# Kernel tuning notes

Measured on AMD Instinct MI355X. Metric: run time of the kernel, lower is better.

## Reference

```python
import jax, jax.numpy as jnp
import numpy as np


def setup_inputs() -> dict:
    key = jax.random.key(0)
    ks = jax.random.split(key, 7)
    B, EN, DE, E, U, T = 8, 512, 64, 512, 512, 100  # batch, max_words, max_label, emb, units, topics
    return {
        "en_seq": jax.random.normal(ks[0], (B, EN, E), dtype=jnp.float32),
        "de_seq": jax.random.normal(ks[1], (B, DE, E), dtype=jnp.float32),
        "topics": jax.random.uniform(ks[2], (B, T), dtype=jnp.float32),
        "w_en": jax.random.normal(ks[3], (E, U), dtype=jnp.float32) * 0.05,
        "w_de": jax.random.normal(ks[4], (E, U), dtype=jnp.float32) * 0.05,
        "nu": jax.random.normal(ks[5], (U,), dtype=jnp.float32) * 0.05,
        "wt": jax.random.normal(ks[6], (E, T), dtype=jnp.float32) * 0.05,
    }


def reference(en_seq, de_seq, topics, w_en, w_de, nu, wt):
    # Additive (Bahdanau-style) attention with a per-batch topic bias.
    att_en = jnp.einsum("bie,eu->biu", en_seq, w_en)        # [B, EN, U]
    att_de = jnp.einsum("bje,eu->bju", de_seq, w_de)        # [B, DE, U]
    topics_w = jnp.einsum("bt,ut->bu", topics, wt)          # [B, U] (wt is [E,U-dim? no: E==U])
    # co_m[b, j, i, u] = att_en[b,i,u] + att_de[b,j,u] + topics_w[b,u]
    co_m = jnp.tanh(att_en[:, None, :, :] + att_de[:, :, None, :]
                    + topics_w[:, None, None, :])           # [B, DE, EN, U]
    mu = jnp.einsum("bjiu,u->bji", co_m, nu)                # [B, DE, EN]
    alphas = jax.nn.softmax(mu, axis=-1)                    # softmax over encoder positions
    p_gen = jax.nn.sigmoid(mu)
    sum_en = jnp.einsum("bji,bie->bje", alphas, en_seq)     # attention-weighted encoder sum
    output = de_seq + sum_en
    return (output, alphas, p_gen)
```

## Files before the change

### kernel.cpp

```cpp
#include <hip/hip_runtime.h>
#include <hip/hip_bf16.h>

#define NB  8
#define ENW 512
#define DEW 64
#define EMB 512
#define UN  512
#define NT  100

#define KSCALE 2.8853900817779268f
#define L2E    1.4426950408889634f

typedef short bf16x8 __attribute__((ext_vector_type(8)));
typedef unsigned short u16x8 __attribute__((ext_vector_type(8)));
typedef float f32x4  __attribute__((ext_vector_type(4)));

__device__ __forceinline__ unsigned short f2bf(float f) {
    union { float f; unsigned int u; } v; v.f = f;
    unsigned int r = v.u + 0x7FFFu + ((v.u >> 16) & 1u);
    return (unsigned short)(r >> 16);
}

__device__ __forceinline__ float rlane(float v, int l) {
    return __int_as_float(__builtin_amdgcn_readlane(__float_as_int(v), l));
}

__global__ __launch_bounds__(256) void prep_kernel(const float* __restrict__ w_en,
                                                   const float* __restrict__ w_de,
                                                   const float* __restrict__ en,
                                                   const float* __restrict__ de,
                                                   const float* __restrict__ topics,
                                                   const float* __restrict__ wt_mat,
                                                   const float* __restrict__ nu,
                                                   unsigned short* __restrict__ wen_t,
                                                   unsigned short* __restrict__ wde_t,
                                                   unsigned short* __restrict__ en_bf,
                                                   unsigned short* __restrict__ de_bf,
                                                   float* __restrict__ tw2,
                                                   float* __restrict__ snu,
                                                   float* __restrict__ nu2) {
    const int bx = blockIdx.x, t = threadIdx.x;
    if (bx < 128) {
        __shared__ float tile[64][65];
        const float* w = (bx < 64) ? w_en : w_de;
        unsigned short* o = (bx < 64) ? wen_t : wde_t;
        const int tb = bx & 63;
        const int r0 = (tb >> 3) * 64;
        const int c0 = (tb & 7) * 64;
        const int rr = t >> 4, cc = (t & 15) * 4;
#pragma unroll
        for (int q = 0; q < 4; ++q) {
            float4 v = *(const float4*)(w + (size_t)(r0 + rr + 16 * q) * 512 + c0 + cc);
            *(float4*)&tile[rr + 16 * q][cc] = v;
        }
        __syncthreads();
#pragma unroll
        for (int q = 0; q < 4; ++q) {
            int ul = rr + 16 * q;
            int el = cc;
            ushort4 v;
            v.x = f2bf(KSCALE * tile[el][ul]);
            v.y = f2bf(KSCALE * tile[el + 1][ul]);
            v.z = f2bf(KSCALE * tile[el + 2][ul]);
            v.w = f2bf(KSCALE * tile[el + 3][ul]);
            *(ushort4*)(o + (size_t)(c0 + ul) * 512 + r0 + el) = v;
        }
    } else if (bx < 1280) {
        const bool is_en = (bx < 1152);
        const float* src = is_en ? en : de;
        unsigned short* dst = is_en ? en_bf : de_bf;
        const int idx = ((is_en ? (bx - 128) : (bx - 1152)) * 256 + t) * 8;
        float4 a0 = *(const float4*)(src + idx);
        float4 a1 = *(const float4*)(src + idx + 4);
        u16x8 o;
        o[0] = f2bf(a0.x); o[1] = f2bf(a0.y); o[2] = f2bf(a0.z); o[3] = f2bf(a0.w);
        o[4] = f2bf(a1.x); o[5] = f2bf(a1.y); o[6] = f2bf(a1.z); o[7] = f2bf(a1.w);
        *(u16x8*)(dst + idx) = o;
    } else if (bx < 1296) {
        int idx = (bx - 1280) * 256 + t;
        int b = idx >> 9, u = idx & 511;
        const float* tp = topics + b * NT;
        const float* wp = wt_mat + u * NT;
        float s = 0.f;
        for (int tt = 0; tt < NT; ++tt) s += tp[tt] * wp[tt];
        tw2[idx] = KSCALE * s;
    } else {
        __shared__ float red[256];
        float n0 = nu[t], n1 = nu[t + 256];
        nu2[t] = -2.f * n0;
        nu2[t + 256] = -2.f * n1;
        red[t] = n0 + n1;
        __syncthreads();
        for (int off = 128; off > 0; off >>= 1) {
            if (t < off) red[t] += red[t + off];
            __syncthreads();
        }
        if (t == 0) snu[0] = red[0];
    }
}

__global__ __launch_bounds__(256) void gemm_fused(const unsigned short* __restrict__ en_bf,
                                                  const unsigned short* __restrict__ de_bf,
                                                  const unsigned short* __restrict__ wen_t,
                                                  const unsigned short* __restrict__ wde_t,
                                                  const float* __restrict__ tw2,
                                                  float* __restrict__ att_en2,
                                                  float* __restrict__ bias2) {
    const int K = 512, N = 512;
    const int bx = blockIdx.x;
    const bool is_de = (bx >= 64);
    const unsigned short* A = is_de ? de_bf : en_bf;
    const unsigned short* Bt = is_de ? wde_t : wen_t;
    float* C = is_de ? bias2 : att_en2;
    const int mb = is_de ? (bx - 64) : bx;

    const int lane = threadIdx.x & 63;
    const int wave = threadIdx.x >> 6;
    const int m0 = mb * 64 + wave * 16;
    const int n0 = blockIdx.y * 64;
    const int row = m0 + (lane & 15);
    const int kq  = (lane >> 4) * 8;

    f32x4 acc[4];
#pragma unroll
    for (int nn = 0; nn < 4; ++nn) acc[nn] = 0.f;

    const unsigned short* ap = A + (size_t)row * K + kq;
    const unsigned short* bp = Bt + (size_t)(n0 + (lane & 15)) * K + kq;
#pragma unroll 4
    for (int kc = 0; kc < K; kc += 32) {
        bf16x8 a = *(const bf16x8*)(ap + kc);
#pragma unroll
        for (int nn = 0; nn < 4; ++nn) {
            bf16x8 b = *(const bf16x8*)(bp + (size_t)nn * 16 * K + kc);
            acc[nn] = __builtin_amdgcn_mfma_f32_16x16x32_bf16(a, b, acc[nn], 0, 0, 0);
        }
    }
    const int crow = m0 + (lane >> 4) * 4;
    const int ccol = lane & 15;
#pragma unroll
    for (int nn = 0; nn < 4; ++nn)
#pragma unroll
        for (int r = 0; r < 4; ++r) {
            int rw = crow + r, cl = n0 + nn * 16 + ccol;
            float v = acc[nn][r];
            if (is_de) v += tw2[(rw >> 6) * 512 + cl];
            C[(size_t)rw * N + cl] = v;
        }
}

__global__ __launch_bounds__(256) void mu3_kernel(const float* __restrict__ att_en2,
                                                  const float* __restrict__ bias2,
                                                  const float* __restrict__ nu2,
                                                  const float* __restrict__ snu,
                                                  float* __restrict__ mu) {
    __shared__ float As[16][132];
    __shared__ float Bs[16][132];
    __shared__ float Ns[128];
    const int t = threadIdx.x;
    const int bx = blockIdx.x;
    const int jg = bx & 3;
    const int isplit = (bx >> 2) & 31;
    const int b = bx >> 7;
    const int i0 = isplit * 16, j0 = jg * 16;
    const int il = t & 15, jr = t >> 4;

    const float* aeb = att_en2 + (size_t)(b * ENW + i0) * UN;
    const float* bib = bias2 + (size_t)(b * DEW + j0) * UN;

    float s0 = 0.f, s1 = 0.f;
    for (int uc = 0; uc < 512; uc += 128) {
#pragma unroll
        for (int q = 0; q < 2; ++q) {
            int idx = q * 256 + t;
            int row = idx >> 5, c4 = idx & 31;
            float4 va = *(const float4*)(aeb + (size_t)row * UN + uc + c4 * 4);
            *(float4*)&As[row][c4 * 4] = va;
            float4 vb = *(const float4*)(bib + (size_t)row * UN + uc + c4 * 4);
            *(float4*)&Bs[row][c4 * 4] = vb;
        }
        if (t < 32) *(float4*)&Ns[t * 4] = *(const float4*)(nu2 + uc + t * 4);
        __syncthreads();
#pragma unroll 8
        for (int c = 0; c < 32; ++c) {
            float4 a  = *(const float4*)&As[il][c * 4];
            float4 bb = *(const float4*)&Bs[jr][c * 4];
            float4 nv = *(const float4*)&Ns[c * 4];
            float e0 = __builtin_amdgcn_exp2f(a.x + bb.x);
            float e1 = __builtin_amdgcn_exp2f(a.y + bb.y);
            float e2 = __builtin_amdgcn_exp2f(a.z + bb.z);
            float e3 = __builtin_amdgcn_exp2f(a.w + bb.w);
            s0 = fmaf(nv.x, __builtin_amdgcn_rcpf(e0 + 1.f), s0);
            s1 = fmaf(nv.y, __builtin_amdgcn_rcpf(e1 + 1.f), s1);
            s0 = fmaf(nv.z, __builtin_amdgcn_rcpf(e2 + 1.f), s0);
            s1 = fmaf(nv.w, __builtin_amdgcn_rcpf(e3 + 1.f), s1);
        }
        __syncthreads();
    }
    mu[(size_t)(b * DEW + j0 + jr) * ENW + i0 + il] = snu[0] + s0 + s1;
}

__global__ __launch_bounds__(256) void softmax_kernel(const float* __restrict__ mu,
                                                      float* __restrict__ alphas,
                                                      float* __restrict__ p_gen) {
    const int bj = blockIdx.x;
    const float* mup = mu + (size_t)bj * ENW;
    const int t = threadIdx.x;
    float v0 = mup[t], v1 = mup[t + 256];

    float m = fmaxf(v0, v1);
#pragma unroll
    for (int off = 32; off > 0; off >>= 1) m = fmaxf(m, __shfl_xor(m, off));
    __shared__ float wmax[4];
    if ((t & 63) == 0) wmax[t >> 6] = m;
    __syncthreads();
    m = fmaxf(fmaxf(wmax[0], wmax[1]), fmaxf(wmax[2], wmax[3]));

    float e0 = __builtin_amdgcn_exp2f((v0 - m) * L2E);
    float e1 = __builtin_amdgcn_exp2f((v1 - m) * L2E);
    float s = e0 + e1;
#pragma unroll
    for (int off = 32; off > 0; off >>= 1) s += __shfl_xor(s, off);
    __shared__ float wsum[4];
    if ((t & 63) == 0) wsum[t >> 6] = s;
    __syncthreads();
    s = wsum[0] + wsum[1] + wsum[2] + wsum[3];
    float inv = __builtin_amdgcn_rcpf(s);

    alphas[(size_t)bj * ENW + t]       = e0 * inv;
    alphas[(size_t)bj * ENW + t + 256] = e1 * inv;
    p_gen[(size_t)bj * ENW + t]        = __builtin_amdgcn_rcpf(1.f + __builtin_amdgcn_exp2f(-v0 * L2E));
    p_gen[(size_t)bj * ENW + t + 256]  = __builtin_amdgcn_rcpf(1.f + __builtin_amdgcn_exp2f(-v1 * L2E));
}

__global__ __launch_bounds__(64) void outsum_kernel(const float* __restrict__ alphas,
                                                    const float* __restrict__ en,
                                                    float* __restrict__ partial) {
    const int bx = blockIdx.x;
    const int iq = bx & 3;
    const int eh = (bx >> 2) & 1;
    const int jq = (bx >> 3) & 15;
    const int b  = bx >> 7;
    const int lane = threadIdx.x;
    const int i0 = iq * 128, j0 = jq * 4;

    float2 av[4];
#pragma unroll
    for (int jj = 0; jj < 4; ++jj)
        av[jj] = *(const float2*)(alphas + (size_t)(b * DEW + j0 + jj) * ENW + i0 + lane * 2);

    const float* enb = en + (size_t)b * ENW * EMB + eh * 256 + lane * 4;
    f32x4 acc[4];
#pragma unroll
    for (int jj = 0; jj < 4; ++jj) acc[jj] = 0.f;

#pragma unroll 4
    for (int k2 = 0; k2 < 64; ++k2) {
        float4 x0 = *(const float4*)(enb + (size_t)(i0 + 2 * k2) * EMB);
        float4 x1 = *(const float4*)(enb + (size_t)(i0 + 2 * k2 + 1) * EMB);
#pragma unroll
        for (int jj = 0; jj < 4; ++jj) {
            float w0 = rlane(av[jj].x, k2);
            float w1 = rlane(av[jj].y, k2);
            acc[jj][0] = fmaf(w0, x0.x, fmaf(w1, x1.x, acc[jj][0]));
            acc[jj][1] = fmaf(w0, x0.y, fmaf(w1, x1.y, acc[jj][1]));
            acc[jj][2] = fmaf(w0, x0.z, fmaf(w1, x1.z, acc[jj][2]));
            acc[jj][3] = fmaf(w0, x0.w, fmaf(w1, x1.w, acc[jj][3]));
        }
    }
#pragma unroll
    for (int jj = 0; jj < 4; ++jj) {
        float* pp = partial + (size_t)iq * 262144
                  + (size_t)(b * DEW + j0 + jj) * EMB + eh * 256 + lane * 4;
        *(f32x4*)pp = acc[jj];
    }
}

__global__ __launch_bounds__(256) void finout_kernel(const float* __restrict__ partial,
                                                     const float* __restrict__ de,
                                                     float* __restrict__ out) {
    const int idx = (blockIdx.x * 256 + threadIdx.x) * 4;
    float4 d  = *(const float4*)(de + idx);
    float4 p0 = *(const float4*)(partial + idx);
    float4 p1 = *(const float4*)(partial + 262144 + idx);
    float4 p2 = *(const float4*)(partial + 524288 + idx);
    float4 p3 = *(const float4*)(partial + 786432 + idx);
    float4 o;
    o.x = d.x + (p0.x + p1.x) + (p2.x + p3.x);
    o.y = d.y + (p0.y + p1.y) + (p2.y + p3.y);
    o.z = d.z + (p0.z + p1.z) + (p2.z + p3.z);
    o.w = d.w + (p0.w + p1.w) + (p2.w + p3.w);
    *(float4*)(out + idx) = o;
}

extern "C" void kernel_launch(void* const* d_in, const int* in_sizes, int n_in,
                              void* d_out, int out_size, void* d_ws, size_t ws_size,
                              hipStream_t stream) {
    const float* en     = (const float*)d_in[0];
    const float* de     = (const float*)d_in[1];
    const float* topics = (const float*)d_in[2];
    const float* w_en   = (const float*)d_in[3];
    const float* w_de   = (const float*)d_in[4];
    const float* nu     = (const float*)d_in[5];
    const float* wt     = (const float*)d_in[6];

    float* out    = (float*)d_out;
    float* alphas = out + 262144;
    float* p_gen  = out + 524288;

    char* ws = (char*)d_ws;
    float* att_en2        = (float*)(ws);
    float* bias2          = (float*)(ws + 8388608);
    float* tw2            = (float*)(ws + 9437184);
    float* mu             = (float*)(ws + 9453568);
    unsigned short* en_bf = (unsigned short*)(ws + 10502144);
    unsigned short* de_bf = (unsigned short*)(ws + 14696448);
    unsigned short* wen_t = (unsigned short*)(ws + 15220736);
    unsigned short* wde_t = (unsigned short*)(ws + 15745024);
    float* snu            = (float*)(ws + 16269312);
    float* nu2            = (float*)(ws + 16269328);
    float* partial        = (float*)(ws + 16777216);

    prep_kernel<<<1297, 256, 0, stream>>>(w_en, w_de, en, de, topics, wt, nu,
                                          wen_t, wde_t, en_bf, de_bf, tw2, snu, nu2);
    gemm_fused<<<dim3(72, 8), 256, 0, stream>>>(en_bf, de_bf, wen_t, wde_t, tw2,
                                                att_en2, bias2);
    mu3_kernel<<<1024, 256, 0, stream>>>(att_en2, bias2, nu2, snu, mu);
    softmax_kernel<<<512, 256, 0, stream>>>(mu, alphas, p_gen);
    outsum_kernel<<<1024, 64, 0, stream>>>(alphas, en, partial);
    finout_kernel<<<256, 256, 0, stream>>>(partial, de, out);
}
```

Before: 150.0 us.

## Factor exp out of mu inner loop and fuse softmax with weighted sum

The GEMM epilogue now stores exp2 of the scaled projections, so the mu inner loop evaluates tanh through exp(a)*exp(b)+1 with one FMA instead of an add and an exp per element. Softmax, p_gen, the alpha-weighted encoder sum and the de_seq residual are merged into one kernel that keeps alphas in shared memory, which removes the partial buffer and two launches. The factored exponentials can overflow to inf for large inputs, but rcp of inf still gives the correct limit. The fused kernel launches only 256 blocks, so there is less parallelism in the weighted-sum stage.

New measurement: 141.4 us. 1.06x faster.

```diff
diff --git a/kernel.cpp b/kernel.cpp
--- a/kernel.cpp
+++ b/kernel.cpp
@@ -104,14 +104,14 @@
                                                   const unsigned short* __restrict__ wen_t,
                                                   const unsigned short* __restrict__ wde_t,
                                                   const float* __restrict__ tw2,
-                                                  float* __restrict__ att_en2,
-                                                  float* __restrict__ bias2) {
+                                                  float* __restrict__ Ea,
+                                                  float* __restrict__ Eb) {
     const int K = 512, N = 512;
     const int bx = blockIdx.x;
     const bool is_de = (bx >= 64);
     const unsigned short* A = is_de ? de_bf : en_bf;
     const unsigned short* Bt = is_de ? wde_t : wen_t;
-    float* C = is_de ? bias2 : att_en2;
+    float* C = is_de ? Eb : Ea;
     const int mb = is_de ? (bx - 64) : bx;
 
     const int lane = threadIdx.x & 63;
@@ -145,12 +145,12 @@
             int rw = crow + r, cl = n0 + nn * 16 + ccol;
             float v = acc[nn][r];
             if (is_de) v += tw2[(rw >> 6) * 512 + cl];
-            C[(size_t)rw * N + cl] = v;
-        }
-}
-
-__global__ __launch_bounds__(256) void mu3_kernel(const float* __restrict__ att_en2,
-                                                  const float* __restrict__ bias2,
+            C[(size_t)rw * N + cl] = __builtin_amdgcn_exp2f(v);
+        }
+}
+
+__global__ __launch_bounds__(256) void mu4_kernel(const float* __restrict__ Ea,
+                                                  const float* __restrict__ Eb,
                                                   const float* __restrict__ nu2,
                                                   const float* __restrict__ snu,
                                                   float* __restrict__ mu) {
@@ -165,8 +165,8 @@
     const int i0 = isplit * 16, j0 = jg * 16;
     const int il = t & 15, jr = t >> 4;
 
-    const float* aeb = att_en2 + (size_t)(b * ENW + i0) * UN;
-    const float* bib = bias2 + (size_t)(b * DEW + j0) * UN;
+    const float* aeb = Ea + (size_t)(b * ENW + i0) * UN;
+    const float* bib = Eb + (size_t)(b * DEW + j0) * UN;
 
     float s0 = 0.f, s1 = 0.f;
     for (int uc = 0; uc < 512; uc += 128) {
@@ -186,111 +186,118 @@
             float4 a  = *(const float4*)&As[il][c * 4];
             float4 bb = *(const float4*)&Bs[jr][c * 4];
             float4 nv = *(const float4*)&Ns[c * 4];
-            float e0 = __builtin_amdgcn_exp2f(a.x + bb.x);
-            float e1 = __builtin_amdgcn_exp2f(a.y + bb.y);
-            float e2 = __builtin_amdgcn_exp2f(a.z + bb.z);
-            float e3 = __builtin_amdgcn_exp2f(a.w + bb.w);
-            s0 = fmaf(nv.x, __builtin_amdgcn_rcpf(e0 + 1.f), s0);
-            s1 = fmaf(nv.y, __builtin_amdgcn_rcpf(e1 + 1.f), s1);
-            s0 = fmaf(nv.z, __builtin_amdgcn_rcpf(e2 + 1.f), s0);
-            s1 = fmaf(nv.w, __builtin_amdgcn_rcpf(e3 + 1.f), s1);
+            float e0 = fmaf(a.x, bb.x, 1.f);
+            float e1 = fmaf(a.y, bb.y, 1.f);
+            float e2 = fmaf(a.z, bb.z, 1.f);
+            float e3 = fmaf(a.w, bb.w, 1.f);
+            s0 = fmaf(nv.x, __builtin_amdgcn_rcpf(e0), s0);
+            s1 = fmaf(nv.y, __builtin_amdgcn_rcpf(e1), s1);
+            s0 = fmaf(nv.z, __builtin_amdgcn_rcpf(e2), s0);
+            s1 = fmaf(nv.w, __builtin_amdgcn_rcpf(e3), s1);
         }
         __syncthreads();
     }
     mu[(size_t)(b * DEW + j0 + jr) * ENW + i0 + il] = snu[0] + s0 + s1;
 }
 
-__global__ __launch_bounds__(256) void softmax_kernel(const float* __restrict__ mu,
+__global__ __launch_bounds__(256) void softfin_kernel(const float* __restrict__ mu,
+                                                      const float* __restrict__ en,
+                                                      const float* __restrict__ de,
+                                                      float* __restrict__ out,
                                                       float* __restrict__ alphas,
                                                       float* __restrict__ p_gen) {
-    const int bj = blockIdx.x;
-    const float* mup = mu + (size_t)bj * ENW;
+    __shared__ float Al[4][512];
+    __shared__ float Ps[4][4][256];
+    const int bx = blockIdx.x;
+    const int eh = bx & 1;
+    const int jq = (bx >> 1) & 15;
+    const int b  = bx >> 5;
     const int t = threadIdx.x;
-    float v0 = mup[t], v1 = mup[t + 256];
-
-    float m = fmaxf(v0, v1);
-#pragma unroll
-    for (int off = 32; off > 0; off >>= 1) m = fmaxf(m, __shfl_xor(m, off));
-    __shared__ float wmax[4];
-    if ((t & 63) == 0) wmax[t >> 6] = m;
+    const int wave = t >> 6, lane = t & 63;
+    const int j0 = jq * 4;
+
+    {
+        const int bj = b * DEW + j0 + wave;
+        const float* mup = mu + (size_t)bj * ENW;
+        float v[8], a[8];
+#pragma unroll
+        for (int c = 0; c < 8; ++c) v[c] = mup[c * 64 + lane];
+        float mx = v[0];
+#pragma unroll
+        for (int c = 1; c < 8; ++c) mx = fmaxf(mx, v[c]);
+#pragma unroll
+        for (int off = 32; off > 0; off >>= 1) mx = fmaxf(mx, __shfl_xor(mx, off));
+        float s = 0.f;
+#pragma unroll
+        for (int c = 0; c < 8; ++c) { a[c] = __builtin_amdgcn_exp2f((v[c] - mx) * L2E); s += a[c]; }
+#pragma unroll
+        for (int off = 32; off > 0; off >>= 1) s += __shfl_xor(s, off);
+        float inv = __builtin_amdgcn_rcpf(s);
+#pragma unroll
+        for (int c = 0; c < 8; ++c) {
+            a[c] *= inv;
+            Al[wave][c * 64 + lane] = a[c];
+        }
+        if (eh == 0) {
+            float* alp = alphas + (size_t)bj * ENW;
+            float* pgp = p_gen + (size_t)bj * ENW;
+#pragma unroll
+            for (int c = 0; c < 8; ++c) {
+                alp[c * 64 + lane] = a[c];
+                pgp[c * 64 + lane] = __builtin_amdgcn_rcpf(1.f + __builtin_amdgcn_exp2f(-v[c] * L2E));
+            }
+        }
+    }
     __syncthreads();
-    m = fmaxf(fmaxf(wmax[0], wmax[1]), fmaxf(wmax[2], wmax[3]));
-
-    float e0 = __builtin_amdgcn_exp2f((v0 - m) * L2E);
-    float e1 = __builtin_amdgcn_exp2f((v1 - m) * L2E);
-    float s = e0 + e1;
-#pragma unroll
-    for (int off = 32; off > 0; off >>= 1) s += __shfl_xor(s, off);
-    __shared__ float wsum[4];
-    if ((t & 63) == 0) wsum[t >> 6] = s;
-    __syncthreads();
-    s = wsum[0] + wsum[1] + wsum[2] + wsum[3];
-    float inv = __builtin_amdgcn_rcpf(s);
-
-    alphas[(size_t)bj * ENW + t]       = e0 * inv;
-    alphas[(size_t)bj * ENW + t + 256] = e1 * inv;
-    p_gen[(size_t)bj * ENW + t]        = __builtin_amdgcn_rcpf(1.f + __builtin_amdgcn_exp2f(-v0 * L2E));
-    p_gen[(size_t)bj * ENW + t + 256]  = __builtin_amdgcn_rcpf(1.f + __builtin_amdgcn_exp2f(-v1 * L2E));
-}
-
-__global__ __launch_bounds__(64) void outsum_kernel(const float* __restrict__ alphas,
-                                                    const float* __restrict__ en,
-                                                    float* __restrict__ partial) {
-    const int bx = blockIdx.x;
-    const int iq = bx & 3;
-    const int eh = (bx >> 2) & 1;
-    const int jq = (bx >> 3) & 15;
-    const int b  = bx >> 7;
-    const int lane = threadIdx.x;
-    const int i0 = iq * 128, j0 = jq * 4;
-
-    float2 av[4];
-#pragma unroll
-    for (int jj = 0; jj < 4; ++jj)
-        av[jj] = *(const float2*)(alphas + (size_t)(b * DEW + j0 + jj) * ENW + i0 + lane * 2);
-
+
+    const int i0 = wave * 128;
     const float* enb = en + (size_t)b * ENW * EMB + eh * 256 + lane * 4;
     f32x4 acc[4];
 #pragma unroll
     for (int jj = 0; jj < 4; ++jj) acc[jj] = 0.f;
-
-#pragma unroll 4
-    for (int k2 = 0; k2 < 64; ++k2) {
-        float4 x0 = *(const float4*)(enb + (size_t)(i0 + 2 * k2) * EMB);
-        float4 x1 = *(const float4*)(enb + (size_t)(i0 + 2 * k2 + 1) * EMB);
-#pragma unroll
-        for (int jj = 0; jj < 4; ++jj) {
-            float w0 = rlane(av[jj].x, k2);
-            float w1 = rlane(av[jj].y, k2);
-            acc[jj][0] = fmaf(w0, x0.x, fmaf(w1, x1.x, acc[jj][0]));
-            acc[jj][1] = fmaf(w0, x0.y, fmaf(w1, x1.y, acc[jj][1]));
-            acc[jj][2] = fmaf(w0, x0.z, fmaf(w1, x1.z, acc[jj][2]));
-            acc[jj][3] = fmaf(w0, x0.w, fmaf(w1, x1.w, acc[jj][3]));
-        }
-    }
-#pragma unroll
-    for (int jj = 0; jj < 4; ++jj) {
-        float* pp = partial + (size_t)iq * 262144
-                  + (size_t)(b * DEW + j0 + jj) * EMB + eh * 256 + lane * 4;
-        *(f32x4*)pp = acc[jj];
-    }
-}
-
-__global__ __launch_bounds__(256) void finout_kernel(const float* __restrict__ partial,
-                                                     const float* __restrict__ de,
-                                                     float* __restrict__ out) {
-    const int idx = (blockIdx.x * 256 + threadIdx.x) * 4;
-    float4 d  = *(const float4*)(de + idx);
-    float4 p0 = *(const float4*)(partial + idx);
-    float4 p1 = *(const float4*)(partial + 262144 + idx);
-    float4 p2 = *(const float4*)(partial + 524288 + idx);
-    float4 p3 = *(const float4*)(partial + 786432 + idx);
-    float4 o;
-    o.x = d.x + (p0.x + p1.x) + (p2.x + p3.x);
-    o.y = d.y + (p0.y + p1.y) + (p2.y + p3.y);
-    o.z = d.z + (p0.z + p1.z) + (p2.z + p3.z);
-    o.w = d.w + (p0.w + p1.w) + (p2.w + p3.w);
-    *(float4*)(out + idx) = o;
+    for (int ig = 0; ig < 128; ig += 4) {
+        const int ib = i0 + ig;
+        float4 al0 = *(const float4*)&Al[0][ib];
+        float4 al1 = *(const float4*)&Al[1][ib];
+        float4 al2 = *(const float4*)&Al[2][ib];
+        float4 al3 = *(const float4*)&Al[3][ib];
+#pragma unroll
+        for (int r = 0; r < 4; ++r) {
+            float4 x = *(const float4*)(enb + (size_t)(ib + r) * EMB);
+            float w0 = (r == 0) ? al0.x : (r == 1) ? al0.y : (r == 2) ? al0.z : al0.w;
+            float w1 = (r == 0) ? al1.x : (r == 1) ? al1.y : (r == 2) ? al1.z : al1.w;
+            float w2 = (r == 0) ? al2.x : (r == 1) ? al2.y : (r == 2) ? al2.z : al2.w;
+            float w3 = (r == 0) ? al3.x : (r == 1) ? al3.y : (r == 2) ? al3.z : al3.w;
+            acc[0][0] = fmaf(w0, x.x, acc[0][0]); acc[0][1] = fmaf(w0, x.y, acc[0][1]);
+            acc[0][2] = fmaf(w0, x.z, acc[0][2]); acc[0][3] = fmaf(w0, x.w, acc[0][3]);
+            acc[1][0] = fmaf(w1, x.x, acc[1][0]); acc[1][1] = fmaf(w1, x.y, acc[1][1]);
+            acc[1][2] = fmaf(w1, x.z, acc[1][2]); acc[1][3] = fmaf(w1, x.w, acc[1][3]);
+            acc[2][0] = fmaf(w2, x.x, acc[2][0]); acc[2][1] = fmaf(w2, x.y, acc[2][1]);
+            acc[2][2] = fmaf(w2, x.z, acc[2][2]); acc[2][3] = fmaf(w2, x.w, acc[2][3]);
+            acc[3][0] = fmaf(w3, x.x, acc[3][0]); acc[3][1] = fmaf(w3, x.y, acc[3][1]);
+            acc[3][2] = fmaf(w3, x.z, acc[3][2]); acc[3][3] = fmaf(w3, x.w, acc[3][3]);
+        }
+    }
+#pragma unroll
+    for (int jj = 0; jj < 4; ++jj)
+        *(f32x4*)&Ps[wave][jj][lane * 4] = acc[jj];
+    __syncthreads();
+
+    {
+        const int bj = b * DEW + j0 + wave;
+        const int e = eh * 256 + lane * 4;
+        float4 p0 = *(const float4*)&Ps[0][wave][lane * 4];
+        float4 p1 = *(const float4*)&Ps[1][wave][lane * 4];
+        float4 p2 = *(const float4*)&Ps[2][wave][lane * 4];
+        float4 p3 = *(const float4*)&Ps[3][wave][lane * 4];
+        float4 d = *(const float4*)(de + (size_t)bj * EMB + e);
+        float4 o;
+        o.x = d.x + (p0.x + p1.x) + (p2.x + p3.x);
+        o.y = d.y + (p0.y + p1.y) + (p2.y + p3.y);
+        o.z = d.z + (p0.z + p1.z) + (p2.z + p3.z);
+        o.w = d.w + (p0.w + p1.w) + (p2.w + p3.w);
+        *(float4*)(out + (size_t)bj * EMB + e) = o;
+    }
 }
 
 extern "C" void kernel_launch(void* const* d_in, const int* in_sizes, int n_in,
@@ -309,8 +316,8 @@
     float* p_gen  = out + 524288;
 
     char* ws = (char*)d_ws;
-    float* att_en2        = (float*)(ws);
-    float* bias2          = (float*)(ws + 8388608);
+    float* Ea             = (float*)(ws);
+    float* Eb             = (float*)(ws + 8388608);
     float* tw2            = (float*)(ws + 9437184);
     float* mu             = (float*)(ws + 9453568);
     unsigned short* en_bf = (unsigned short*)(ws + 10502144);
@@ -319,14 +326,10 @@
     unsigned short* wde_t = (unsigned short*)(ws + 15745024);
     float* snu            = (float*)(ws + 16269312);
     float* nu2            = (float*)(ws + 16269328);
-    float* partial        = (float*)(ws + 16777216);
 
     prep_kernel<<<1297, 256, 0, stream>>>(w_en, w_de, en, de, topics, wt, nu,
                                           wen_t, wde_t, en_bf, de_bf, tw2, snu, nu2);
-    gemm_fused<<<dim3(72, 8), 256, 0, stream>>>(en_bf, de_bf, wen_t, wde_t, tw2,
-                                                att_en2, bias2);
-    mu3_kernel<<<1024, 256, 0, stream>>>(att_en2, bias2, nu2, snu, mu);
-    softmax_kernel<<<512, 256, 0, stream>>>(mu, alphas, p_gen);
-    outsum_kernel<<<1024, 64, 0, stream>>>(alphas, en, partial);
-    finout_kernel<<<256, 256, 0, stream>>>(partial, de, out);
-}
+    gemm_fused<<<dim3(72, 8), 256, 0, stream>>>(en_bf, de_bf, wen_t, wde_t, tw2, Ea, Eb);
+    mu4_kernel<<<1024, 256, 0, stream>>>(Ea, Eb, nu2, snu, mu);
+    softfin_kernel<<<256, 256, 0, stream>>>(mu, en, de, out, alphas, p_gen);
+}
```
